# Optimization experiments

Hardware: AMD Instinct MI355X
Metric: run time of the kernel (lower is better)

## Reference

```python
import jax, jax.numpy as jnp
import numpy as np

SEQ_LEN = 2048
EMBED = 1024
HIDDEN = 1024
BATCH = 4


def setup_inputs() -> dict:
    key = jax.random.key(0)
    ks = jax.random.split(key, 7)
    # xavier_uniform for weights: limit = sqrt(6/(fan_in+fan_out))
    lim = float(np.sqrt(6.0 / (EMBED + HIDDEN)))
    blim = float(1.0 / np.sqrt(EMBED))  # torch Linear default bias init U(-1/sqrt(fan_in), ...)
    inputs = jax.random.normal(ks[0], (BATCH, SEQ_LEN, EMBED), dtype=jnp.float32)
    Wq = jax.random.uniform(ks[1], (HIDDEN, EMBED), jnp.float32, -lim, lim)
    Wk = jax.random.uniform(ks[2], (HIDDEN, EMBED), jnp.float32, -lim, lim)
    Wv = jax.random.uniform(ks[3], (HIDDEN, EMBED), jnp.float32, -lim, lim)
    bq = jax.random.uniform(ks[4], (HIDDEN,), jnp.float32, -blim, blim)
    bk = jax.random.uniform(ks[5], (HIDDEN,), jnp.float32, -blim, blim)
    bv = jax.random.uniform(ks[6], (HIDDEN,), jnp.float32, -blim, blim)
    return {"inputs": inputs, "Wq": Wq, "bq": bq, "Wk": Wk, "bk": bk, "Wv": Wv, "bv": bv}


def reference(inputs, Wq, bq, Wk, bk, Wv, bv):
    B, S, E = inputs.shape
    q = jnp.einsum('bse,he->bsh', inputs, Wq) + bq  # [B,S,H]
    k = jnp.einsum('bse,he->bsh', inputs, Wk) + bk
    v = jnp.einsum('bse,he->bsh', inputs, Wv) + bv
    # NOTE: source scales by 1/sqrt(embed_size), not hidden_size
    scores = jnp.einsum('bqh,bkh->bqk', q, k) / jnp.sqrt(jnp.float32(E))
    causal = jnp.tril(jnp.ones((S, S), dtype=bool))  # [S,S]
    scores = jnp.where(causal[None, :, :], scores, -jnp.inf)
    attn = jax.nn.softmax(scores, axis=-1)
    return jnp.einsum('bqk,bkh->bqh', attn, v)
```

## Files before the change

kernel.cpp:

```cpp
#include <hip/hip_runtime.h>
#include <cstdint>
#include <cstddef>
#include <math.h>

typedef unsigned short u16;

#define S_LEN 2048
#define EMB   1024
#define HID   1024
#define NB    4

using bf16x8 = __attribute__((ext_vector_type(8))) __bf16;
using f32x4  = __attribute__((ext_vector_type(4))) float;


__device__ __forceinline__ u16 f2bf(float f) {
  union { float f; uint32_t u; } c; c.f = f;
  uint32_t u = c.u;
  uint32_t r = (u + 0x7fffu + ((u >> 16) & 1u)) >> 16;
  return (u16)r;
}

__device__ __forceinline__ float bf2f(uint32_t hi16) {
  union { uint32_t u; float f; } c; c.u = hi16;
  return c.f;
}

__device__ __forceinline__ void gld_lds16(const u16* g, u16* l) {
  auto gp = (const __attribute__((address_space(1))) uint32_t*)(uintptr_t)(const void*)g;
  auto lp = (__attribute__((address_space(3))) uint32_t*)(uintptr_t)(void*)l;
  __builtin_amdgcn_global_load_lds(gp, lp, 16, 0, 0);
}


__global__ void cvt_all(const float* __restrict__ x,  const float* __restrict__ wq,
                        const float* __restrict__ wk, const float* __restrict__ wv,
                        u16* __restrict__ xb, u16* __restrict__ wb, int nx4, int nw4lg2) {
  const int nw4 = 1 << nw4lg2;
  const int total = nx4 + 3 * nw4;
  int i = blockIdx.x * blockDim.x + threadIdx.x;
  const int stride = gridDim.x * blockDim.x;
  for (; i < total; i += stride) {
    const float* src; u16* dst; int j;
    if (i < nx4) { src = x; dst = xb; j = i; }
    else {
      const int k = i - nx4;
      const int wsel = k >> nw4lg2;
      j = k & (nw4 - 1);
      src = (wsel == 0) ? wq : (wsel == 1) ? wk : wv;
      dst = wb + ((size_t)wsel << (nw4lg2 + 2));
    }
    float4 v = reinterpret_cast<const float4*>(src)[j];
    reinterpret_cast<ushort4*>(dst)[j] =
      make_ushort4(f2bf(v.x), f2bf(v.y), f2bf(v.z), f2bf(v.w));
  }
}


template<int EPI>
__global__ __launch_bounds__(256, 2)
void gemmT(const u16* __restrict__ A, const u16* __restrict__ Bw, void* __restrict__ Cv,
           const float* __restrict__ b0, const float* __restrict__ b1,
           const float* __restrict__ b2, u16* __restrict__ VT,
           int N, long sA, long sB, long sC, float scale)
{
  constexpr int K = 1024;
  constexpr int NTILE = K / 64;
  const int z = blockIdx.z;
  A  += (long)z * sA;
  Bw += (long)z * sB;

  __shared__ __align__(16) u16 smem[32768];

  const int tid = threadIdx.x;
  const int l   = tid & 63;
  const int w   = tid >> 6;
  const int wr  = w >> 1;
  const int wc  = w & 1;

  int bm, bn;
  if constexpr (EPI == 2) {
    const int x0 = blockIdx.x;
    const int x  = (x0 & 7) * ((int)gridDim.x >> 3) + (x0 >> 3);
    int bi = (int)((sqrtf(8.0f * (float)x + 1.0f) - 1.0f) * 0.5f);
    while ((bi + 1) * (bi + 2) / 2 <= x) ++bi;
    while (bi * (bi + 1) / 2 > x) --bi;
    bm = bi * 128;
    bn = (x - bi * (bi + 1) / 2) * 128;
  } else {
    const int nwg = gridDim.x * gridDim.y;
    const int lin = blockIdx.y * gridDim.x + blockIdx.x;
    const int sw  = (lin & 7) * (nwg >> 3) + (lin >> 3);
    bm = (sw / gridDim.x) * 128;
    bn = (sw % gridDim.x) * 128;
  }

  const int arow = w * 16 + (l >> 2);
  const int acs  = (l & 3) ^ (((l >> 5) & 1) << 1);
  const u16* gbA  = A  + (long)(bm + arow) * K + acs * 8;
  const u16* gbA2 = gbA + 64L * K;
  const u16* gbB  = Bw + (long)(bn + arow) * K + acs * 8;
  const u16* gbB2 = gbB + 64L * K;

#define STGH(t, s, dbase)                                                       \
  do {                                                                          \
    const long _o = (long)(t) * 64 + (s) * 32;                                  \
    gld_lds16(gbA  + _o, smem + (dbase) + (s) * 4096 +        w * 512);         \
    gld_lds16(gbA2 + _o, smem + (dbase) + (s) * 4096 + 2048 + w * 512);         \
    gld_lds16(gbB  + _o, smem + (dbase) + 8192 + (s) * 4096 +        w * 512);  \
    gld_lds16(gbB2 + _o, smem + (dbase) + 8192 + (s) * 4096 + 2048 + w * 512);  \
  } while (0)

  const int lr  = l & 15;
  const int kg  = l >> 4;
  const int kgp = kg ^ (((lr >> 3) & 1) << 1);
  int aoff[4], boff[4];
#pragma unroll
  for (int m = 0; m < 4; ++m) aoff[m] = (wr * 64 + m * 16 + lr) * 32 + kgp * 8;
#pragma unroll
  for (int n = 0; n < 4; ++n) boff[n] = (wc * 64 + n * 16 + lr) * 32 + kgp * 8;

  f32x4 acc[4][4] = {};
  bf16x8 Ea[4], Eb[4], Oa[4], Ob[4];

  STGH(0, 0, 0);
  STGH(0, 1, 0);
  asm volatile("s_waitcnt vmcnt(0)" ::: "memory");
  __builtin_amdgcn_s_barrier();
  asm volatile("" ::: "memory");
#pragma unroll
  for (int m_ = 0; m_ < 4; ++m_)
    Ea[m_] = *reinterpret_cast<const bf16x8*>(smem + aoff[m_]);
#pragma unroll
  for (int n_ = 0; n_ < 4; ++n_)
    Eb[n_] = *reinterpret_cast<const bf16x8*>(smem + 8192 + boff[n_]);

#define PHASE(STGSTMT, dR, sR, Fa, Fb, Ca, Cb)                                  \
  do {                                                                          \
    STGSTMT;                                                                    \
    asm volatile("s_waitcnt vmcnt(4)" ::: "memory");                            \
    __builtin_amdgcn_s_barrier();                                               \
    asm volatile("" ::: "memory");                                              \
    __builtin_amdgcn_s_setprio(1);                                              \
    _Pragma("unroll")                                                           \
    for (int m_ = 0; m_ < 4; ++m_)                                              \
      _Pragma("unroll")                                                         \
      for (int n_ = 0; n_ < 4; ++n_)                                            \
        acc[m_][n_] = __builtin_amdgcn_mfma_f32_16x16x32_bf16(                  \
            Ca[m_], Cb[n_], acc[m_][n_], 0, 0, 0);                              \
    __builtin_amdgcn_s_setprio(0);                                              \
    asm volatile("" ::: "memory");                                              \
    {                                                                           \
      const u16* hA = smem + (dR) * 16384 + (sR) * 4096;                        \
      const u16* hB = smem + (dR) * 16384 + 8192 + (sR) * 4096;                 \
      _Pragma("unroll")                                                         \
      for (int m_ = 0; m_ < 4; ++m_)                                            \
        Fa[m_] = *reinterpret_cast<const bf16x8*>(hA + aoff[m_]);               \
      _Pragma("unroll")                                                         \
      for (int n_ = 0; n_ < 4; ++n_)                                            \
        Fb[n_] = *reinterpret_cast<const bf16x8*>(hB + boff[n_]);               \
    }                                                                           \
  } while (0)

#pragma unroll 1
  for (int i = 0; i < NTILE / 2; ++i) {
    const int t1 = 2 * i + 1;
    const int t2 = (2 * i + 2 < NTILE) ? 2 * i + 2 : NTILE - 1;
    PHASE(STGH(t1, 0, 16384), 0, 1, Oa, Ob, Ea, Eb);
    PHASE(STGH(t1, 1, 16384), 1, 0, Ea, Eb, Oa, Ob);
    PHASE(STGH(t2, 0, 0),     1, 1, Oa, Ob, Ea, Eb);
    PHASE(STGH(t2, 1, 0),     0, 0, Ea, Eb, Oa, Ob);
  }
#undef PHASE
#undef STGH

  if constexpr (EPI == 2) {
    u16* C = (u16*)Cv + (long)z * sC;
#pragma unroll
    for (int n = 0; n < 4; ++n) {
      const int col = bn + wc * 64 + n * 16 + lr;
#pragma unroll
      for (int m = 0; m < 4; ++m) {
        const int row0 = bm + wr * 64 + m * 16 + kg * 4;
#pragma unroll
        for (int q = 0; q < 4; ++q) {
          const int row = row0 + q;
          float v = acc[m][n][q] * scale;
          if (col > row) v = -1e30f;
          C[(long)row * N + col] = f2bf(v);
        }
      }
    }
  } else {
    constexpr long M = (long)NB * S_LEN;
    const int sel = bn >> 10;
    const float* bias = (sel == 0) ? b0 : (sel == 1) ? b1 : b2;
    u16* QK = (u16*)Cv;
#pragma unroll
    for (int n = 0; n < 4; ++n) {
      const int col = bn + wc * 64 + n * 16 + lr;
      const int h   = col & (HID - 1);
      const float bbv = bias[h];
#pragma unroll
      for (int m = 0; m < 4; ++m) {
        const int row0 = bm + wr * 64 + m * 16 + kg * 4;
        if (sel < 2) {
          u16* dst = QK + (long)sel * M * HID + (long)row0 * HID + h;
#pragma unroll
          for (int q = 0; q < 4; ++q)
            dst[(long)q * HID] = f2bf(acc[m][n][q] + bbv);
        } else {
          const int b = row0 >> 11;
          const int s = row0 & (S_LEN - 1);
          ushort4 o = make_ushort4(f2bf(acc[m][n][0] + bbv), f2bf(acc[m][n][1] + bbv),
                                   f2bf(acc[m][n][2] + bbv), f2bf(acc[m][n][3] + bbv));
          *reinterpret_cast<ushort4*>(VT + ((long)b * HID + h) * S_LEN + s) = o;
        }
      }
    }
  }
}


__global__ __launch_bounds__(512, 2)
void gemm_pv(const u16* __restrict__ Pm, const u16* __restrict__ VTm, float* __restrict__ Cm)
{
  const int z = blockIdx.z;
  const u16* A = Pm  + (long)z * S_LEN * S_LEN;
  const u16* B = VTm + (long)z * HID * S_LEN;
  float*    Cz = Cm  + (long)z * S_LEN * HID;

  __shared__ __align__(16) u16 smem[32768];

  const int tid = threadIdx.x;
  const int l   = tid & 63;
  const int w   = tid >> 6;
  const int wr  = w >> 2;
  const int wc  = w & 3;
  const int bn  = blockIdx.x * 128;
  const int pr  = blockIdx.y;

  const int lr  = l & 15;
  const int kg  = l >> 4;
  const int kgp = kg ^ (((lr >> 3) & 1) << 1);
  int aoff[4], boff[2];
#pragma unroll
  for (int m = 0; m < 4; ++m) aoff[m] = (wr * 64 + m * 16 + lr) * 32 + kgp * 8;
#pragma unroll
  for (int n = 0; n < 2; ++n) boff[n] = (wc * 32 + n * 16 + lr) * 32 + kgp * 8;

  const int arow = w * 16 + (l >> 2);
  const int acs  = (l & 3) ^ (((l >> 5) & 1) << 1);

#pragma unroll 1
  for (int it = 0; it < 2; ++it) {
    const int bi = (it == 0) ? (15 - pr) : pr;
    const int bm = bi * 128;
    const int NTILE = (bi + 1) * 2;

    const u16* gbA = A + (long)(bm + arow) * S_LEN + acs * 8;
    const u16* gbB = B + (long)(bn + arow) * S_LEN + acs * 8;

#define STGH(t, s, dbase)                                                       \
  do {                                                                          \
    const long _o = (long)(t) * 64 + (s) * 32;                                  \
    gld_lds16(gbA + _o, smem + (dbase) + (s) * 4096 + w * 512);                 \
    gld_lds16(gbB + _o, smem + (dbase) + 8192 + (s) * 4096 + w * 512);          \
  } while (0)

    if (it) {
      __builtin_amdgcn_s_barrier();
      asm volatile("" ::: "memory");
    }

    f32x4 acc[4][2] = {};

    STGH(0, 0, 0);
    STGH(0, 1, 0);
    asm volatile("s_waitcnt vmcnt(0)" ::: "memory");
    __builtin_amdgcn_s_barrier();
    asm volatile("" ::: "memory");

#define PHASE(d, s, STGSTMT)                                                    \
  do {                                                                          \
    const u16* hA = smem + (d) * 16384 + (s) * 4096;                            \
    const u16* hB = smem + (d) * 16384 + 8192 + (s) * 4096;                     \
    bf16x8 av[4], bv[2];                                                        \
    _Pragma("unroll")                                                           \
    for (int m_ = 0; m_ < 4; ++m_)                                              \
      av[m_] = *reinterpret_cast<const bf16x8*>(hA + aoff[m_]);                 \
    _Pragma("unroll")                                                           \
    for (int n_ = 0; n_ < 2; ++n_)                                              \
      bv[n_] = *reinterpret_cast<const bf16x8*>(hB + boff[n_]);                 \
    STGSTMT;                                                                    \
    asm volatile("s_waitcnt vmcnt(2)" ::: "memory");                            \
    __builtin_amdgcn_s_barrier();                                               \
    asm volatile("" ::: "memory");                                              \
    __builtin_amdgcn_s_setprio(1);                                              \
    _Pragma("unroll")                                                           \
    for (int m_ = 0; m_ < 4; ++m_)                                              \
      _Pragma("unroll")                                                         \
      for (int n_ = 0; n_ < 2; ++n_)                                            \
        acc[m_][n_] = __builtin_amdgcn_mfma_f32_16x16x32_bf16(                  \
            av[m_], bv[n_], acc[m_][n_], 0, 0, 0);                              \
    __builtin_amdgcn_s_setprio(0);                                              \
    asm volatile("" ::: "memory");                                              \
  } while (0)

#pragma unroll 1
    for (int i = 0; i < NTILE / 2; ++i) {
      const int t1 = 2 * i + 1;
      const int t2 = (2 * i + 2 < NTILE) ? 2 * i + 2 : NTILE - 1;
      PHASE(0, 0, STGH(t1, 0, 16384));
      PHASE(0, 1, STGH(t1, 1, 16384));
      PHASE(1, 0, STGH(t2, 0, 0));
      PHASE(1, 1, STGH(t2, 1, 0));
    }
#undef PHASE
#undef STGH

#pragma unroll
    for (int n = 0; n < 2; ++n) {
      const int col = bn + wc * 32 + n * 16 + lr;
#pragma unroll
      for (int m = 0; m < 4; ++m) {
        const int row0 = bm + wr * 64 + m * 16 + kg * 4;
#pragma unroll
        for (int q = 0; q < 4; ++q)
          Cz[(long)(row0 + q) * HID + col] = acc[m][n][q];
      }
    }
  }
}


__global__ __launch_bounds__(256)
void softmax_causal(const u16* __restrict__ Sc, u16* __restrict__ P, long sS, long sP)
{
  const int row  = blockIdx.x;
  const int z    = blockIdx.y;
  const int kend = ((row >> 7) + 1) << 7;
  const u16* srow = Sc + (long)z * sS + (long)row * S_LEN;
  u16*      prow = P  + (long)z * sP + (long)row * S_LEN;
  const int t = threadIdx.x;
  const int lane = t & 63, wave = t >> 6;

  const bool p0 = (8 * t) < kend;

  float e[8];
  float mx = -1e30f;
  if (p0) {
    uint4 u = reinterpret_cast<const uint4*>(srow)[t];
    uint32_t wv[4] = {u.x, u.y, u.z, u.w};
#pragma unroll
    for (int i = 0; i < 4; ++i) {
      const float lo = bf2f((wv[i] & 0xffffu) << 16);
      const float hi = bf2f(wv[i] & 0xffff0000u);
      e[2 * i]     = lo;
      e[2 * i + 1] = hi;
      mx = fmaxf(mx, fmaxf(lo, hi));
    }
  }

  __shared__ float red[8];
#pragma unroll
  for (int off = 32; off; off >>= 1) mx = fmaxf(mx, __shfl_down(mx, off));
  if (lane == 0) red[wave] = mx;
  __syncthreads();
  mx = fmaxf(fmaxf(red[0], red[1]), fmaxf(red[2], red[3]));

  float sm = 0.0f;
  if (p0) {
#pragma unroll
    for (int i = 0; i < 8; ++i) e[i] = __expf(e[i] - mx);
    sm = ((e[0] + e[1]) + (e[2] + e[3])) + ((e[4] + e[5]) + (e[6] + e[7]));
  }
#pragma unroll
  for (int off = 32; off; off >>= 1) sm += __shfl_down(sm, off);
  if (lane == 0) red[4 + wave] = sm;
  __syncthreads();
  sm = (red[4] + red[5]) + (red[6] + red[7]);

  const float inv = 1.0f / sm;
  if (p0) {
    uint32_t o[4];
#pragma unroll
    for (int i = 0; i < 4; ++i) {
      const uint32_t a = f2bf(e[2 * i] * inv);
      const uint32_t b = f2bf(e[2 * i + 1] * inv);
      o[i] = a | (b << 16);
    }
    reinterpret_cast<uint4*>(prow)[t] = make_uint4(o[0], o[1], o[2], o[3]);
  }
}


extern "C" void kernel_launch(void* const* d_in, const int* in_sizes, int n_in,
                              void* d_out, int out_size, void* d_ws, size_t ws_size,
                              hipStream_t stream)
{
  const float* x  = (const float*)d_in[0];
  const float* Wq = (const float*)d_in[1];
  const float* bq = (const float*)d_in[2];
  const float* Wk = (const float*)d_in[3];
  const float* bk = (const float*)d_in[4];
  const float* Wv = (const float*)d_in[5];
  const float* bv = (const float*)d_in[6];
  float* out = (float*)d_out;

  const long M = (long)NB * S_LEN;

  u16* xb  = (u16*)d_ws;
  u16* wqb = xb  + M * EMB;
  u16* Qb  = wqb + 3L * HID * EMB;
  u16* Kb  = Qb  + M * HID;
  u16* VT  = Kb  + M * HID;
  char* rest = (char*)(VT + M * HID);
  const size_t used  = (size_t)(rest - (char*)d_ws);
  const size_t ssz   = (size_t)S_LEN * S_LEN;
  const size_t need4 = used + (size_t)NB * ssz * 2 * 2;
  const int nb = (ws_size >= need4) ? NB : 1;
  u16* scores = (u16*)rest;
  u16* P      = scores + (size_t)nb * ssz;

  cvt_all<<<2048, 256, 0, stream>>>(x, Wq, Wk, Wv, xb, wqb, (int)(M * EMB / 4), 18);

  gemmT<4><<<dim3(24, 64, 1), 256, 0, stream>>>(xb, wqb, Qb, bq, bk, bv, VT,
                                                3 * HID, 0, 0, 0, 1.0f);

  const float scale = 0.03125f;
  const int TRI = 16 * 17 / 2;

  if (nb == NB) {
    dim3 gs(TRI, 1, NB);
    gemmT<2><<<gs, 256, 0, stream>>>(Qb, Kb, scores, nullptr, nullptr, nullptr, nullptr,
                                     S_LEN, (long)S_LEN * HID, (long)S_LEN * HID,
                                     (long)ssz, scale);
    softmax_causal<<<dim3(S_LEN, NB), 256, 0, stream>>>(scores, P, (long)ssz, (long)ssz);
    gemm_pv<<<dim3(8, 8, NB), 512, 0, stream>>>(P, VT, out);
  } else {
    for (int b = 0; b < NB; ++b) {
      const u16* Qbb = Qb + (long)b * S_LEN * HID;
      const u16* Kbb = Kb + (long)b * S_LEN * HID;
      const u16* VTb = VT + (long)b * HID * S_LEN;
      float* outb = out + (long)b * S_LEN * HID;
      dim3 gs(TRI, 1, 1);
      gemmT<2><<<gs, 256, 0, stream>>>(Qbb, Kbb, scores, nullptr, nullptr, nullptr, nullptr,
                                       S_LEN, 0, 0, 0, scale);
      softmax_causal<<<dim3(S_LEN, 1), 256, 0, stream>>>(scores, P, 0, 0);
      gemm_pv<<<dim3(8, 8, 1), 512, 0, stream>>>(P, VTb, outb);
    }
  }
}
```

Baseline: 158.7 us.

## Replace double-buffered GEMM pipeline with five-slot ring buffer and deeper prefetch

Restructures the bf16 GEMM main loop from a two-stage double buffer with register ping-pong into a five-slot LDS ring of 32-wide K halves. Global-to-LDS loads are issued three steps ahead and waited with vmcnt(8). The aim is to hide more global-load latency behind the MFMA work. In exchange LDS use grows from 64KB to 80KB per block, which may reduce occupancy below the launch bound of two blocks. LDS reads now happen right before each MFMA step rather than overlapping with the previous one.

```diff
diff --git a/kernel.cpp b/kernel.cpp
--- a/kernel.cpp
+++ b/kernel.cpp
@@ -64,13 +64,13 @@
            const float* __restrict__ b2, u16* __restrict__ VT,
            int N, long sA, long sB, long sC, float scale)
 {
-  constexpr int K = 1024;
-  constexpr int NTILE = K / 64;
+  constexpr int K  = 1024;
+  constexpr int NH = K / 32;
   const int z = blockIdx.z;
   A  += (long)z * sA;
   Bw += (long)z * sB;
 
-  __shared__ __align__(16) u16 smem[32768];
+  __shared__ __align__(16) u16 smem[40960];
 
   const int tid = threadIdx.x;
   const int l   = tid & 63;
@@ -102,13 +102,13 @@
   const u16* gbB  = Bw + (long)(bn + arow) * K + acs * 8;
   const u16* gbB2 = gbB + 64L * K;
 
-#define STGH(t, s, dbase)                                                       \
+#define STGH(h, rb)                                                             \
   do {                                                                          \
-    const long _o = (long)(t) * 64 + (s) * 32;                                  \
-    gld_lds16(gbA  + _o, smem + (dbase) + (s) * 4096 +        w * 512);         \
-    gld_lds16(gbA2 + _o, smem + (dbase) + (s) * 4096 + 2048 + w * 512);         \
-    gld_lds16(gbB  + _o, smem + (dbase) + 8192 + (s) * 4096 +        w * 512);  \
-    gld_lds16(gbB2 + _o, smem + (dbase) + 8192 + (s) * 4096 + 2048 + w * 512);  \
+    const long _o = (long)(h) * 32;                                             \
+    gld_lds16(gbA  + _o, smem + (rb) +        w * 512);                         \
+    gld_lds16(gbA2 + _o, smem + (rb) + 2048 + w * 512);                         \
+    gld_lds16(gbB  + _o, smem + (rb) + 4096 +        w * 512);                  \
+    gld_lds16(gbB2 + _o, smem + (rb) + 4096 + 2048 + w * 512);                  \
   } while (0)
 
   const int lr  = l & 15;
@@ -118,60 +118,52 @@
 #pragma unroll
   for (int m = 0; m < 4; ++m) aoff[m] = (wr * 64 + m * 16 + lr) * 32 + kgp * 8;
 #pragma unroll
-  for (int n = 0; n < 4; ++n) boff[n] = (wc * 64 + n * 16 + lr) * 32 + kgp * 8;
+  for (int n = 0; n < 4; ++n) boff[n] = 4096 + (wc * 64 + n * 16 + lr) * 32 + kgp * 8;
 
   f32x4 acc[4][4] = {};
-  bf16x8 Ea[4], Eb[4], Oa[4], Ob[4];
-
-  STGH(0, 0, 0);
-  STGH(0, 1, 0);
+
+  STGH(0, 2 * 8192);
+  STGH(1, 3 * 8192);
+  STGH(2, 4 * 8192);
   asm volatile("s_waitcnt vmcnt(0)" ::: "memory");
   __builtin_amdgcn_s_barrier();
   asm volatile("" ::: "memory");
-#pragma unroll
-  for (int m_ = 0; m_ < 4; ++m_)
-    Ea[m_] = *reinterpret_cast<const bf16x8*>(smem + aoff[m_]);
-#pragma unroll
-  for (int n_ = 0; n_ < 4; ++n_)
-    Eb[n_] = *reinterpret_cast<const bf16x8*>(smem + 8192 + boff[n_]);
-
-#define PHASE(STGSTMT, dR, sR, Fa, Fb, Ca, Cb)                                  \
-  do {                                                                          \
-    STGSTMT;                                                                    \
-    asm volatile("s_waitcnt vmcnt(4)" ::: "memory");                            \
-    __builtin_amdgcn_s_barrier();                                               \
-    asm volatile("" ::: "memory");                                              \
-    __builtin_amdgcn_s_setprio(1);                                              \
-    _Pragma("unroll")                                                           \
-    for (int m_ = 0; m_ < 4; ++m_)                                              \
-      _Pragma("unroll")                                                         \
-      for (int n_ = 0; n_ < 4; ++n_)                                            \
-        acc[m_][n_] = __builtin_amdgcn_mfma_f32_16x16x32_bf16(                  \
-            Ca[m_], Cb[n_], acc[m_][n_], 0, 0, 0);                              \
-    __builtin_amdgcn_s_setprio(0);                                              \
-    asm volatile("" ::: "memory");                                              \
-    {                                                                           \
-      const u16* hA = smem + (dR) * 16384 + (sR) * 4096;                        \
-      const u16* hB = smem + (dR) * 16384 + 8192 + (sR) * 4096;                 \
-      _Pragma("unroll")                                                         \
-      for (int m_ = 0; m_ < 4; ++m_)                                            \
-        Fa[m_] = *reinterpret_cast<const bf16x8*>(hA + aoff[m_]);               \
-      _Pragma("unroll")                                                         \
-      for (int n_ = 0; n_ < 4; ++n_)                                            \
-        Fb[n_] = *reinterpret_cast<const bf16x8*>(hB + boff[n_]);               \
-    }                                                                           \
-  } while (0)
+
+  int rd = 2;
+  int st = 0;
 
 #pragma unroll 1
-  for (int i = 0; i < NTILE / 2; ++i) {
-    const int t1 = 2 * i + 1;
-    const int t2 = (2 * i + 2 < NTILE) ? 2 * i + 2 : NTILE - 1;
-    PHASE(STGH(t1, 0, 16384), 0, 1, Oa, Ob, Ea, Eb);
-    PHASE(STGH(t1, 1, 16384), 1, 0, Ea, Eb, Oa, Ob);
-    PHASE(STGH(t2, 0, 0),     1, 1, Oa, Ob, Ea, Eb);
-    PHASE(STGH(t2, 1, 0),     0, 0, Ea, Eb, Oa, Ob);
-  }
-#undef PHASE
+  for (int p = 0; p < NH; ++p) {
+    const int h  = (p + 3 < NH) ? p + 3 : NH - 1;
+    const u16* hR = smem + rd * 8192;
+
+    bf16x8 av[4], bv[4];
+#pragma unroll
+    for (int m_ = 0; m_ < 4; ++m_)
+      av[m_] = *reinterpret_cast<const bf16x8*>(hR + aoff[m_]);
+#pragma unroll
+    for (int n_ = 0; n_ < 4; ++n_)
+      bv[n_] = *reinterpret_cast<const bf16x8*>(hR + boff[n_]);
+
+    STGH(h, st * 8192);
+
+    asm volatile("s_waitcnt vmcnt(8)" ::: "memory");
+    __builtin_amdgcn_s_barrier();
+    asm volatile("" ::: "memory");
+
+    __builtin_amdgcn_s_setprio(1);
+#pragma unroll
+    for (int m_ = 0; m_ < 4; ++m_)
+#pragma unroll
+      for (int n_ = 0; n_ < 4; ++n_)
+        acc[m_][n_] = __builtin_amdgcn_mfma_f32_16x16x32_bf16(
+            av[m_], bv[n_], acc[m_][n_], 0, 0, 0);
+    __builtin_amdgcn_s_setprio(0);
+    asm volatile("" ::: "memory");
+
+    rd = (rd == 4) ? 0 : rd + 1;
+    st = (st == 4) ? 0 : st + 1;
+  }
 #undef STGH
 
   if constexpr (EPI == 2) {
```

After: 160.4 us. No clear change (+1.1%).
